# Optimization experiments

Hardware: AMD Instinct MI355X
Metric: run time of the kernel (lower is better)

The kernel has to match this reference:

```python
import jax, jax.numpy as jnp
import numpy as np

NA, NW = 131072, 131072
N = NA + NW
E = 1048576
R = 4
DIN = 64
H = 128
L = 2
EPS = 1e-5


def setup_inputs() -> dict:
    key = jax.random.key(0)
    ks = jax.random.split(key, 20)
    s_in = 1.0 / np.sqrt(DIN)
    s_h = 1.0 / np.sqrt(H)
    return {
        "x_assignments": jax.random.normal(ks[0], (NA, DIN), jnp.float32),
        "x_workers": jax.random.normal(ks[1], (NW, DIN), jnp.float32),
        "edge_index": jax.random.randint(ks[2], (2, E), 0, N),
        "edge_type": jax.random.randint(ks[3], (E,), 0, R),
        "W_in_a": jax.random.normal(ks[4], (DIN, H), jnp.float32) * s_in,
        "b_in_a": jnp.zeros((H,), jnp.float32),
        "W_in_w": jax.random.normal(ks[5], (DIN, H), jnp.float32) * s_in,
        "b_in_w": jnp.zeros((H,), jnp.float32),
        "W_rel": jax.random.normal(ks[6], (L, R, H, H), jnp.float32) * s_h,
        "W_root": jax.random.normal(ks[7], (L, H, H), jnp.float32) * s_h,
        "b_conv": jnp.zeros((L, H), jnp.float32),
        "ln_g": jnp.ones((L, H), jnp.float32),
        "ln_b": jnp.zeros((L, H), jnp.float32),
        "W_out": jax.random.normal(ks[8], (H, 1), jnp.float32) * s_h,
        "b_out": jnp.zeros((1,), jnp.float32),
        "base": jnp.zeros((), jnp.float32),
    }


def _layernorm(x, g, b):
    mu = jnp.mean(x, axis=-1, keepdims=True)
    var = jnp.var(x, axis=-1, keepdims=True)
    return (x - mu) * jax.lax.rsqrt(var + EPS) * g + b


def reference(x_assignments, x_workers, edge_index, edge_type,
              W_in_a, b_in_a, W_in_w, b_in_w,
              W_rel, W_root, b_conv, ln_g, ln_b,
              W_out, b_out, base):
    # type-specific input projection + relu, then flatten node space
    ha = jax.nn.relu(x_assignments @ W_in_a + b_in_a)
    hw = jax.nn.relu(x_workers @ W_in_w + b_in_w)
    h = jnp.concatenate([ha, hw], axis=0)  # [N, H]
    src, dst = edge_index[0], edge_index[1]
    for l in range(L):
        hs = h[src]  # [E, H] gathered source features
        out = h @ W_root[l] + b_conv[l]  # root transform + bias
        for r in range(R):
            m = (edge_type == r).astype(h.dtype)  # [E]
            agg = jax.ops.segment_sum(hs * m[:, None], dst, num_segments=N)
            cnt = jax.ops.segment_sum(m, dst, num_segments=N)
            mean = agg / jnp.maximum(cnt, 1.0)[:, None]  # per-relation mean aggr
            out = out + mean @ W_rel[l, r]
        h = jax.nn.relu(_layernorm(out, ln_g[l], ln_b[l]))
        # dropout inactive (eval mode)
    h_t = h[:NA]  # target node type slice (offset 0)
    pred = base + (h_t @ W_out + b_out)[:, 0]
    return pred
```

## Files before the change

### kernel.cpp

```cpp
#include <hip/hip_runtime.h>

#define NA_ 131072
#define NN  262144
#define EE  1048576
#define RR  4
#define EPS_ 1e-5f

typedef unsigned short ushort_t;
typedef unsigned char uchar_t;
typedef unsigned int uint_t;
typedef __attribute__((ext_vector_type(8))) short bf16x8;
typedef __attribute__((ext_vector_type(4))) float f32x4;

__device__ __forceinline__ float bf2f(uint_t u16) {
    return __uint_as_float(u16 << 16);
}
__device__ __forceinline__ uint_t f2bf(float f) {
    uint_t x = __float_as_uint(f);
    return (x + 0x7fffu + ((x >> 16) & 1u)) >> 16;
}

__device__ __forceinline__ void gl2lds16(const void* g, void* l) {
    __builtin_amdgcn_global_load_lds(
        (const __attribute__((address_space(1))) void*)g,
        (__attribute__((address_space(3))) void*)l, 16, 0, 0);
}
__device__ __forceinline__ void gl2lds16_nt(const void* g, void* l) {
    __builtin_amdgcn_global_load_lds(
        (const __attribute__((address_space(1))) void*)g,
        (__attribute__((address_space(3))) void*)l, 16, 0, 2);
}

__global__ __launch_bounds__(256) void proj_gemm(const float* __restrict__ A,
                                                 const short* __restrict__ Btg,
                                                 const float* __restrict__ bias,
                                                 ushort_t* __restrict__ C) {
    const int K = 64;
    __shared__ short As[128][K + 8];
    __shared__ short Bs[128][K + 8];
    const int tid  = threadIdx.x;
    const int lane = tid & 63;
    const int l15  = lane & 15;
    const int q    = lane >> 4;
    const int wv   = tid >> 6;
    const int wr   = (wv >> 1) * 64;
    const int wc   = (wv & 1) * 64;
    const size_t blockRow = (size_t)blockIdx.x * 128;

    #pragma unroll
    for (int it = 0; it < 4; it++) {
        int sidx = (it * 256 + tid) * 8;
        int row = sidx / K, col = sidx % K;
        const float* Ag = A + (blockRow + row) * K + col;
        float4 v0 = *(const float4*)Ag;
        float4 v1 = *(const float4*)(Ag + 4);
        uint4 u;
        u.x = f2bf(v0.x) | (f2bf(v0.y) << 16);
        u.y = f2bf(v0.z) | (f2bf(v0.w) << 16);
        u.z = f2bf(v1.x) | (f2bf(v1.y) << 16);
        u.w = f2bf(v1.z) | (f2bf(v1.w) << 16);
        *(uint4*)&As[row][col] = u;
        *(uint4*)&Bs[row][col] = *(const uint4*)(Btg + (size_t)row * K + col);
    }
    __syncthreads();

    f32x4 acc[4][4];
    #pragma unroll
    for (int i = 0; i < 4; i++)
        #pragma unroll
        for (int j = 0; j < 4; j++) {
            acc[i][j][0] = 0.f; acc[i][j][1] = 0.f;
            acc[i][j][2] = 0.f; acc[i][j][3] = 0.f;
        }

    #pragma unroll
    for (int kk = 0; kk < 2; kk++) {
        bf16x8 af[4], bfr[4];
        #pragma unroll
        for (int i = 0; i < 4; i++)
            af[i] = *(const bf16x8*)&As[wr + i * 16 + l15][kk * 32 + q * 8];
        #pragma unroll
        for (int j = 0; j < 4; j++)
            bfr[j] = *(const bf16x8*)&Bs[wc + j * 16 + l15][kk * 32 + q * 8];
        #pragma unroll
        for (int i = 0; i < 4; i++)
            #pragma unroll
            for (int j = 0; j < 4; j++)
                acc[i][j] = __builtin_amdgcn_mfma_f32_16x16x32_bf16(
                    af[i], bfr[j], acc[i][j], 0, 0, 0);
    }

    #pragma unroll
    for (int j = 0; j < 4; j++) {
        int gcol = wc + j * 16 + l15;
        float bv = bias[gcol];
        #pragma unroll
        for (int i = 0; i < 4; i++) {
            size_t rbase = blockRow + wr + i * 16 + q * 4;
            #pragma unroll
            for (int r = 0; r < 4; r++) {
                float v = fmaxf(acc[i][j][r] + bv, 0.f);
                C[(rbase + r) * 128 + gcol] = (ushort_t)f2bf(v);
            }
        }
    }
}

__global__ void prep_weights(const float* __restrict__ Wia,
                             const float* __restrict__ Wiw,
                             const float* __restrict__ Wroot,
                             const float* __restrict__ Wrel,
                             short* __restrict__ wt) {
    int e = blockIdx.x * 256 + threadIdx.x;
    if (e < 8192) {
        int k = e >> 7, n = e & 127;
        wt[n * 64 + k] = (short)f2bf(Wia[e]);
    } else if (e < 16384) {
        int t = e - 8192;
        int k = t >> 7, n = t & 127;
        wt[8192 + n * 64 + k] = (short)f2bf(Wiw[t]);
    } else {
        int t = e - 16384;
        int l = t / 81920;
        int d = t % 81920;
        int kc = d / 16384;
        int rem2 = d % 16384;
        int n = rem2 >> 7;
        int kkk = rem2 & 127;
        float val = (kc < 4)
            ? Wrel[(((size_t)l * 4 + kc) * 128 + kkk) * 128 + n]
            : Wroot[((size_t)l * 128 + kkk) * 128 + n];
        wt[16384 + (size_t)l * 81920 + kc * 16384 + n * 128 + kkk] =
            (short)f2bf(val);
    }
}

__global__ void count_edges(const int* __restrict__ dstv,
                            const int* __restrict__ et,
                            uint_t* __restrict__ cntp,
                            uchar_t* __restrict__ rank) {
    int base = blockIdx.x * 1024 + threadIdx.x;
    int e0 = base, e1 = base + 256, e2 = base + 512, e3 = base + 768;
    int r0 = et[e0], r1 = et[e1], r2 = et[e2], r3 = et[e3];
    int d0 = dstv[e0], d1 = dstv[e1], d2 = dstv[e2], d3 = dstv[e3];
    uint_t o0 = atomicAdd(&cntp[(size_t)d0 * 16], 1u << (8 * r0));
    uint_t o1 = atomicAdd(&cntp[(size_t)d1 * 16], 1u << (8 * r1));
    uint_t o2 = atomicAdd(&cntp[(size_t)d2 * 16], 1u << (8 * r2));
    uint_t o3 = atomicAdd(&cntp[(size_t)d3 * 16], 1u << (8 * r3));
    rank[e0] = (uchar_t)((o0 >> (8 * r0)) & 0xffu);
    rank[e1] = (uchar_t)((o1 >> (8 * r1)) & 0xffu);
    rank[e2] = (uchar_t)((o2 >> (8 * r2)) & 0xffu);
    rank[e3] = (uchar_t)((o3 >> (8 * r3)) & 0xffu);
}

__global__ void inv_deg(const uint_t* __restrict__ cntp,
                        float* __restrict__ inv,
                        int* __restrict__ deg,
                        uint_t* __restrict__ prefd) {
    int i = blockIdx.x * 256 + threadIdx.x;
    if (i < NN) {
        uint_t c = cntp[(size_t)i * 16];
        int c0 = c & 255, c1 = (c >> 8) & 255, c2 = (c >> 16) & 255, c3 = c >> 24;
        float4 w;
        w.x = 1.0f / (float)(c0 > 1 ? c0 : 1);
        w.y = 1.0f / (float)(c1 > 1 ? c1 : 1);
        w.z = 1.0f / (float)(c2 > 1 ? c2 : 1);
        w.w = 1.0f / (float)(c3 > 1 ? c3 : 1);
        ((float4*)inv)[i] = w;
        deg[i] = c0 + c1 + c2 + c3;
        prefd[i] = ((uint_t)c0 << 8) | ((uint_t)(c0 + c1) << 16)
                 | ((uint_t)(c0 + c1 + c2) << 24);
    }
}

__global__ void scan1(const int* __restrict__ deg, int* __restrict__ offs,
                      int* __restrict__ bsum) {
    __shared__ int lds[256];
    int tid = threadIdx.x;
    int i = blockIdx.x * 256 + tid;
    int v = deg[i];
    int incl = v;
    lds[tid] = incl;
    __syncthreads();
    for (int off = 1; off < 256; off <<= 1) {
        int t = (tid >= off) ? lds[tid - off] : 0;
        __syncthreads();
        incl += t;
        lds[tid] = incl;
        __syncthreads();
    }
    offs[i] = incl - v;
    if (tid == 255) bsum[blockIdx.x] = incl;
}

__global__ void scan_bsum(int* __restrict__ bsum) {
    __shared__ int lds[256];
    int tid = threadIdx.x;
    int t0 = bsum[tid * 4 + 0], t1 = bsum[tid * 4 + 1];
    int t2 = bsum[tid * 4 + 2], t3 = bsum[tid * 4 + 3];
    int s = t0 + t1 + t2 + t3;
    int incl = s;
    lds[tid] = incl;
    __syncthreads();
    for (int off = 1; off < 256; off <<= 1) {
        int t = (tid >= off) ? lds[tid - off] : 0;
        __syncthreads();
        incl += t;
        lds[tid] = incl;
        __syncthreads();
    }
    int e = incl - s;
    bsum[tid * 4 + 0] = e;
    bsum[tid * 4 + 1] = e + t0;
    bsum[tid * 4 + 2] = e + t0 + t1;
    bsum[tid * 4 + 3] = e + t0 + t1 + t2;
}

__global__ void scan_add(int* __restrict__ offs, const int* __restrict__ bsum) {
    int i = blockIdx.x * 256 + threadIdx.x;
    offs[i] = offs[i] + bsum[blockIdx.x];
    if (i == 0) offs[NN] = EE;
}

__global__ void place_edges(const int* __restrict__ srcv,
                            const int* __restrict__ dstv,
                            const int* __restrict__ et,
                            const uchar_t* __restrict__ rank,
                            const int* __restrict__ offs,
                            const uint_t* __restrict__ prefd,
                            uint_t* __restrict__ pk) {
    int base = blockIdx.x * 1024 + threadIdx.x;
    #pragma unroll
    for (int t = 0; t < 4; t++) {
        int e = base + t * 256;
        int d = dstv[e], r = et[e];
        int pos = offs[d] + (int)((prefd[d] >> (8 * r)) & 255u) + (int)rank[e];
        pk[pos] = (uint_t)srcv[e] | ((uint_t)r << 18);
    }
}

__global__ __launch_bounds__(256) void agg_means(const uint_t* __restrict__ pk,
                                                 const int* __restrict__ offs,
                                                 const ushort_t* __restrict__ hold,
                                                 const float* __restrict__ inv,
                                                 ushort_t* __restrict__ M,
                                                 int lo, int rowsCap) {
    const int wv  = __builtin_amdgcn_readfirstlane(threadIdx.x >> 6);
    const int idx = blockIdx.x * 4 + wv;
    const int d   = lo + idx;
    const int lane = threadIdx.x & 63;
    const int beg = offs[d];
    const int end = offs[d + 1];
    const float4 w4 = ((const float4*)inv)[d];

    float a0x = 0.f, a0y = 0.f, a1x = 0.f, a1y = 0.f;
    float a2x = 0.f, a2y = 0.f, a3x = 0.f, a3y = 0.f;

    const uint_t* hold32 = (const uint_t*)hold;

    auto accs = [&](uint_t p, uint_t v, bool valid) {
        float x = bf2f(v & 0xffffu), y = bf2f(v >> 16);
        uint_t r = p >> 18;
        float m0 = (valid && r == 0u) ? 1.f : 0.f;
        float m1 = (valid && r == 1u) ? 1.f : 0.f;
        float m2 = (valid && r == 2u) ? 1.f : 0.f;
        float m3 = (valid && r == 3u) ? 1.f : 0.f;
        a0x += m0 * x;  a0y += m0 * y;
        a1x += m1 * x;  a1y += m1 * y;
        a2x += m2 * x;  a2y += m2 * y;
        a3x += m3 * x;  a3y += m3 * y;
    };

    for (int e = beg; e < end; e += 8) {
        const int last = end - 1;
        int a1i = (e + 1 < end) ? e + 1 : last;
        int a2i = (e + 2 < end) ? e + 2 : last;
        int a3i = (e + 3 < end) ? e + 3 : last;
        uint_t p0 = pk[e];
        uint_t p1 = pk[a1i];
        uint_t p2 = pk[a2i];
        uint_t p3 = pk[a3i];
        uint_t v0 = hold32[(size_t)(p0 & 0x3FFFFu) * 64 + lane];
        uint_t v1 = hold32[(size_t)(p1 & 0x3FFFFu) * 64 + lane];
        uint_t v2 = hold32[(size_t)(p2 & 0x3FFFFu) * 64 + lane];
        uint_t v3 = hold32[(size_t)(p3 & 0x3FFFFu) * 64 + lane];

        const bool hB = (e + 4 < end);
        if (hB) {
            int b1i = (e + 5 < end) ? e + 5 : last;
            int b2i = (e + 6 < end) ? e + 6 : last;
            int b3i = (e + 7 < end) ? e + 7 : last;
            uint_t q0 = pk[e + 4];
            uint_t q1 = pk[b1i];
            uint_t q2 = pk[b2i];
            uint_t q3 = pk[b3i];
            uint_t u0 = hold32[(size_t)(q0 & 0x3FFFFu) * 64 + lane];
            uint_t u1 = hold32[(size_t)(q1 & 0x3FFFFu) * 64 + lane];
            uint_t u2 = hold32[(size_t)(q2 & 0x3FFFFu) * 64 + lane];
            uint_t u3 = hold32[(size_t)(q3 & 0x3FFFFu) * 64 + lane];
            accs(p0, v0, true);
            accs(p1, v1, true);
            accs(p2, v2, true);
            accs(p3, v3, true);
            accs(q0, u0, true);
            accs(q1, u1, e + 5 < end);
            accs(q2, u2, e + 6 < end);
            accs(q3, u3, e + 7 < end);
        } else {
            accs(p0, v0, true);
            accs(p1, v1, e + 1 < end);
            accs(p2, v2, e + 2 < end);
            accs(p3, v3, e + 3 < end);
        }
    }

    uint_t* P = (uint_t*)M;
    size_t planeU = (size_t)rowsCap * 64;
    size_t rowU = (size_t)idx * 64 + lane;
    __builtin_nontemporal_store(
        f2bf(a0x * w4.x) | (f2bf(a0y * w4.x) << 16), &P[rowU]);
    __builtin_nontemporal_store(
        f2bf(a1x * w4.y) | (f2bf(a1y * w4.y) << 16), &P[planeU + rowU]);
    __builtin_nontemporal_store(
        f2bf(a2x * w4.z) | (f2bf(a2y * w4.z) << 16), &P[2 * planeU + rowU]);
    __builtin_nontemporal_store(
        f2bf(a3x * w4.w) | (f2bf(a3y * w4.w) << 16), &P[3 * planeU + rowU]);
}

template<bool HEAD>
__global__ __launch_bounds__(256) void layer_gemm_ln(
    const ushort_t* __restrict__ Mg,
    const ushort_t* __restrict__ hold,
    const short* __restrict__ Btg,
    const float* __restrict__ bconv,
    const float* __restrict__ lng,
    const float* __restrict__ lnb,
    ushort_t* __restrict__ hnew,
    const float* __restrict__ Wout,
    const float* __restrict__ bout,
    const float* __restrict__ basep,
    float* __restrict__ pred,
    int lo, int rowsCap) {
    __shared__ short As[64 * 128];
    __shared__ short Bs[128 * 128];
    __shared__ float lds_s[64][2], lds_q[64][2], lds_h[64][2];

    const int tid  = threadIdx.x;
    const int lane = tid & 63;
    const int l15  = lane & 15;
    const int q    = lane >> 4;
    const int wv   = tid >> 6;
    const int wr   = (wv >> 1) * 32;
    const int wc   = (wv & 1) * 64;
    const int blockRowL = blockIdx.x * 64;
    const size_t planeS = (size_t)rowsCap * 128;

    f32x4 acc[2][4];
    #pragma unroll
    for (int i = 0; i < 2; i++)
        #pragma unroll
        for (int j = 0; j < 4; j++) {
            acc[i][j][0] = 0.f; acc[i][j][1] = 0.f;
            acc[i][j][2] = 0.f; acc[i][j][3] = 0.f;
        }

    const int rloc = lane >> 4;
    const int gsw  = (lane & 15) ^ ((wv * 4 + rloc) & 15);
    const int lby  = (rloc << 8) + (gsw << 4);

    for (int kc = 0; kc < 5; kc++) {
        const char* asrc = (kc < 4)
            ? (const char*)(Mg + (size_t)kc * planeS + (size_t)blockRowL * 128)
            : (const char*)(hold + (size_t)(lo + blockRowL) * 128);
        const char* bsrc = (const char*)(Btg + (size_t)kc * 16384);
        __syncthreads();
        #pragma unroll
        for (int it = 0; it < 8; it++) {
            int off = it * 4096 + wv * 1024;
            if (it < 4) {
                if (kc < 4) gl2lds16_nt(asrc + off + lby, (char*)As + off);
                else        gl2lds16(asrc + off + lby, (char*)As + off);
            }
            gl2lds16(bsrc + off + lby, (char*)Bs + off);
        }
        __syncthreads();

        #pragma unroll
        for (int kk = 0; kk < 4; kk++) {
            bf16x8 af[2], bfr[4];
            #pragma unroll
            for (int i = 0; i < 2; i++)
                af[i] = *(const bf16x8*)
                    &As[(wr + i * 16 + l15) * 128 + (((kk * 4 + q) ^ l15) << 3)];
            #pragma unroll
            for (int j = 0; j < 4; j++)
                bfr[j] = *(const bf16x8*)
                    &Bs[(wc + j * 16 + l15) * 128 + (((kk * 4 + q) ^ l15) << 3)];
            #pragma unroll
            for (int i = 0; i < 2; i++)
                #pragma unroll
                for (int j = 0; j < 4; j++)
                    acc[i][j] = __builtin_amdgcn_mfma_f32_16x16x32_bf16(
                        af[i], bfr[j], acc[i][j], 0, 0, 0);
        }
    }

    float bj[4], gj[4], bbj[4], wj[4];
    #pragma unroll
    for (int j = 0; j < 4; j++) {
        int col = wc + j * 16 + l15;
        bj[j]  = bconv[col];
        gj[j]  = lng[col];
        bbj[j] = lnb[col];
        if (HEAD) wj[j] = Wout[col];
    }
    #pragma unroll
    for (int i = 0; i < 2; i++)
        #pragma unroll
        for (int j = 0; j < 4; j++)
            #pragma unroll
            for (int r = 0; r < 4; r++) acc[i][j][r] += bj[j];

    float ps[2][4], pq[2][4];
    #pragma unroll
    for (int i = 0; i < 2; i++)
        #pragma unroll
        for (int r = 0; r < 4; r++) {
            float s = 0.f, qq = 0.f;
            #pragma unroll
            for (int j = 0; j < 4; j++) {
                float v = acc[i][j][r];
                s += v;
                qq += v * v;
            }
            ps[i][r] = s;
            pq[i][r] = qq;
        }
    #pragma unroll
    for (int m = 1; m <= 8; m <<= 1)
        #pragma unroll
        for (int i = 0; i < 2; i++)
            #pragma unroll
            for (int r = 0; r < 4; r++) {
                ps[i][r] += __shfl_xor(ps[i][r], m);
                pq[i][r] += __shfl_xor(pq[i][r], m);
            }

    if (l15 == 0) {
        #pragma unroll
        for (int i = 0; i < 2; i++)
            #pragma unroll
            for (int r = 0; r < 4; r++) {
                int row = wr + i * 16 + q * 4 + r;
                lds_s[row][wv & 1] = ps[i][r];
                lds_q[row][wv & 1] = pq[i][r];
            }
    }
    __syncthreads();

    float hs[2][4];
    #pragma unroll
    for (int i = 0; i < 2; i++)
        #pragma unroll
        for (int r = 0; r < 4; r++) {
            int row = wr + i * 16 + q * 4 + r;
            float sum = lds_s[row][0] + lds_s[row][1];
            float sq  = lds_q[row][0] + lds_q[row][1];
            float mu  = sum * (1.0f / 128.0f);
            float var = sq * (1.0f / 128.0f) - mu * mu;
            float rs  = rsqrtf(var + EPS_);
            size_t gr = (size_t)(lo + blockRowL + row) * 128;
            float hd = 0.f;
            #pragma unroll
            for (int j = 0; j < 4; j++) {
                float v = (acc[i][j][r] - mu) * rs * gj[j] + bbj[j];
                v = fmaxf(v, 0.f);
                if (HEAD) hd += v * wj[j];
                else hnew[gr + wc + j * 16 + l15] = (ushort_t)f2bf(v);
            }
            if (HEAD) hs[i][r] = hd;
        }

    if (HEAD) {
        #pragma unroll
        for (int m = 1; m <= 8; m <<= 1)
            #pragma unroll
            for (int i = 0; i < 2; i++)
                #pragma unroll
                for (int r = 0; r < 4; r++)
                    hs[i][r] += __shfl_xor(hs[i][r], m);
        if (l15 == 0) {
            #pragma unroll
            for (int i = 0; i < 2; i++)
                #pragma unroll
                for (int r = 0; r < 4; r++) {
                    int row = wr + i * 16 + q * 4 + r;
                    lds_h[row][wv & 1] = hs[i][r];
                }
        }
        __syncthreads();
        if (tid < 64)
            pred[lo + blockRowL + tid] =
                lds_h[tid][0] + lds_h[tid][1] + bout[0] + basep[0];
    }
}

extern "C" void kernel_launch(void* const* d_in, const int* in_sizes, int n_in,
                              void* d_out, int out_size, void* d_ws, size_t ws_size,
                              hipStream_t stream) {
    const float* x_a    = (const float*)d_in[0];
    const float* x_w    = (const float*)d_in[1];
    const int*   eidx   = (const int*)d_in[2];
    const int*   etype  = (const int*)d_in[3];
    const float* W_in_a = (const float*)d_in[4];
    const float* b_in_a = (const float*)d_in[5];
    const float* W_in_w = (const float*)d_in[6];
    const float* b_in_w = (const float*)d_in[7];
    const float* W_rel  = (const float*)d_in[8];
    const float* W_root = (const float*)d_in[9];
    const float* b_conv = (const float*)d_in[10];
    const float* ln_g   = (const float*)d_in[11];
    const float* ln_b   = (const float*)d_in[12];
    const float* W_out  = (const float*)d_in[13];
    const float* b_out  = (const float*)d_in[14];
    const float* base   = (const float*)d_in[15];

    const int* src  = eidx;
    const int* dstv = eidx + EE;

    char* p = (char*)d_ws;
    auto alloc = [&](size_t bytes) {
        char* q = p;
        p += (bytes + 255) & ~(size_t)255;
        return q;
    };
    ushort_t* hB   = (ushort_t*)alloc((size_t)NN * 128 * 2);
    float*    inv  = (float*)alloc((size_t)RR * NN * 4);
    uint_t*   pk   = (uint_t*)alloc((size_t)EE * 4);
    int*      offs = (int*)alloc((size_t)(NN + 1) * 4);
    short*    wbuf = (short*)alloc((size_t)180224 * 2);
    char*     hA_region = p;
    ushort_t* hA   = (ushort_t*)alloc((size_t)NN * 128 * 2);
    char*     scratch = p;
    uint_t*   cntp  = (uint_t*)alloc((size_t)NN * 64);
    uchar_t*  rank  = (uchar_t*)alloc((size_t)EE);
    int*      deg   = (int*)alloc((size_t)NN * 4);
    uint_t*   prefd = (uint_t*)alloc((size_t)NN * 4);
    int*      bsum  = (int*)alloc((size_t)1024 * 4);

    size_t rem0 = (ws_size > (size_t)(scratch - (char*)d_ws))
                      ? (ws_size - (size_t)(scratch - (char*)d_ws)) : 0;
    int cap0 = (int)(rem0 / 1024);
    if (cap0 > NN) cap0 = NN;
    cap0 &= ~127;
    if (cap0 == 0) cap0 = 128;
    size_t rem1 = (ws_size > (size_t)(hA_region - (char*)d_ws))
                      ? (ws_size - (size_t)(hA_region - (char*)d_ws)) : 0;
    int cap1 = (int)(rem1 / 1024);
    if (cap1 > NA_) cap1 = NA_;
    cap1 &= ~127;
    if (cap1 == 0) cap1 = 128;

    short* wt_ina = wbuf;
    short* wt_inw = wbuf + 8192;
    auto wt_layer = [&](int l) { return wbuf + 16384 + (size_t)l * 81920; };

    hipMemsetAsync(cntp, 0, (size_t)NN * 64, stream);
    count_edges<<<EE / 1024, 256, 0, stream>>>(dstv, etype, cntp, rank);
    inv_deg<<<NN / 256, 256, 0, stream>>>(cntp, inv, deg, prefd);
    scan1<<<NN / 256, 256, 0, stream>>>(deg, offs, bsum);
    scan_bsum<<<1, 256, 0, stream>>>(bsum);
    scan_add<<<NN / 256, 256, 0, stream>>>(offs, bsum);
    place_edges<<<EE / 1024, 256, 0, stream>>>(src, dstv, etype, rank, offs,
                                               prefd, pk);

    prep_weights<<<704, 256, 0, stream>>>(W_in_a, W_in_w, W_root, W_rel, wbuf);

    proj_gemm<<<NA_ / 128, 256, 0, stream>>>(x_a, wt_ina, b_in_a, hA);
    proj_gemm<<<NA_ / 128, 256, 0, stream>>>(x_w, wt_inw, b_in_w,
                                             hA + (size_t)NA_ * 128);

    ushort_t* hc = hA;
    ushort_t* hn = hB;
    for (int l = 0; l < 2; l++) {
        int Nout = (l == 0) ? NN : NA_;
        ushort_t* M = (l == 0) ? (ushort_t*)scratch : (ushort_t*)hA_region;
        int cap = (l == 0) ? cap0 : cap1;
        int nch = (Nout + cap - 1) / cap;
        int chunk = ((Nout / nch) + 127) & ~127;
        if (chunk > cap) chunk = cap;
        for (int lo = 0; lo < Nout; lo += chunk) {
            int cr = (Nout - lo < chunk) ? (Nout - lo) : chunk;
            agg_means<<<cr / 4, 256, 0, stream>>>(pk, offs, hc, inv, M, lo,
                                                  cap);
            if (l == 0)
                layer_gemm_ln<false><<<cr / 64, 256, 0, stream>>>(
                    M, hc, wt_layer(l), b_conv + l * 128, ln_g + l * 128,
                    ln_b + l * 128, hn, nullptr, nullptr, nullptr, nullptr,
                    lo, cap);
            else
                layer_gemm_ln<true><<<cr / 64, 256, 0, stream>>>(
                    M, hc, wt_layer(l), b_conv + l * 128, ln_g + l * 128,
                    ln_b + l * 128, nullptr, W_out, b_out, base,
                    (float*)d_out, lo, cap);
        }
        ushort_t* t = hc; hc = hn; hn = t;
    }
}
```

Measured before the change: 507.6 us.

## Fuse per-relation mean aggregation into layer GEMM+LayerNorm kernel via LDS

Replaces the separate agg_means kernel and its global bf16 M buffer with a fused 1024-thread kernel. Each wave aggregates 4 destination rows into LDS, then the block runs the 5-chunk MFMA GEMM with double-buffered weights and the LayerNorm/head epilogue. This removes the large global write and re-read of the aggregated means and the chunked launch loop. In exchange, LDS use per block rises sharply, limiting occupancy during the latency-bound gather phase.

```diff
diff --git a/kernel.cpp b/kernel.cpp
--- a/kernel.cpp
+++ b/kernel.cpp
@@ -24,11 +24,6 @@
     __builtin_amdgcn_global_load_lds(
         (const __attribute__((address_space(1))) void*)g,
         (__attribute__((address_space(3))) void*)l, 16, 0, 0);
-}
-__device__ __forceinline__ void gl2lds16_nt(const void* g, void* l) {
-    __builtin_amdgcn_global_load_lds(
-        (const __attribute__((address_space(1))) void*)g,
-        (__attribute__((address_space(3))) void*)l, 16, 0, 2);
 }
 
 __global__ __launch_bounds__(256) void proj_gemm(const float* __restrict__ A,
@@ -239,98 +234,12 @@
     }
 }
 
-__global__ __launch_bounds__(256) void agg_means(const uint_t* __restrict__ pk,
-                                                 const int* __restrict__ offs,
-                                                 const ushort_t* __restrict__ hold,
-                                                 const float* __restrict__ inv,
-                                                 ushort_t* __restrict__ M,
-                                                 int lo, int rowsCap) {
-    const int wv  = __builtin_amdgcn_readfirstlane(threadIdx.x >> 6);
-    const int idx = blockIdx.x * 4 + wv;
-    const int d   = lo + idx;
-    const int lane = threadIdx.x & 63;
-    const int beg = offs[d];
-    const int end = offs[d + 1];
-    const float4 w4 = ((const float4*)inv)[d];
-
-    float a0x = 0.f, a0y = 0.f, a1x = 0.f, a1y = 0.f;
-    float a2x = 0.f, a2y = 0.f, a3x = 0.f, a3y = 0.f;
-
-    const uint_t* hold32 = (const uint_t*)hold;
-
-    auto accs = [&](uint_t p, uint_t v, bool valid) {
-        float x = bf2f(v & 0xffffu), y = bf2f(v >> 16);
-        uint_t r = p >> 18;
-        float m0 = (valid && r == 0u) ? 1.f : 0.f;
-        float m1 = (valid && r == 1u) ? 1.f : 0.f;
-        float m2 = (valid && r == 2u) ? 1.f : 0.f;
-        float m3 = (valid && r == 3u) ? 1.f : 0.f;
-        a0x += m0 * x;  a0y += m0 * y;
-        a1x += m1 * x;  a1y += m1 * y;
-        a2x += m2 * x;  a2y += m2 * y;
-        a3x += m3 * x;  a3y += m3 * y;
-    };
-
-    for (int e = beg; e < end; e += 8) {
-        const int last = end - 1;
-        int a1i = (e + 1 < end) ? e + 1 : last;
-        int a2i = (e + 2 < end) ? e + 2 : last;
-        int a3i = (e + 3 < end) ? e + 3 : last;
-        uint_t p0 = pk[e];
-        uint_t p1 = pk[a1i];
-        uint_t p2 = pk[a2i];
-        uint_t p3 = pk[a3i];
-        uint_t v0 = hold32[(size_t)(p0 & 0x3FFFFu) * 64 + lane];
-        uint_t v1 = hold32[(size_t)(p1 & 0x3FFFFu) * 64 + lane];
-        uint_t v2 = hold32[(size_t)(p2 & 0x3FFFFu) * 64 + lane];
-        uint_t v3 = hold32[(size_t)(p3 & 0x3FFFFu) * 64 + lane];
-
-        const bool hB = (e + 4 < end);
-        if (hB) {
-            int b1i = (e + 5 < end) ? e + 5 : last;
-            int b2i = (e + 6 < end) ? e + 6 : last;
-            int b3i = (e + 7 < end) ? e + 7 : last;
-            uint_t q0 = pk[e + 4];
-            uint_t q1 = pk[b1i];
-            uint_t q2 = pk[b2i];
-            uint_t q3 = pk[b3i];
-            uint_t u0 = hold32[(size_t)(q0 & 0x3FFFFu) * 64 + lane];
-            uint_t u1 = hold32[(size_t)(q1 & 0x3FFFFu) * 64 + lane];
-            uint_t u2 = hold32[(size_t)(q2 & 0x3FFFFu) * 64 + lane];
-            uint_t u3 = hold32[(size_t)(q3 & 0x3FFFFu) * 64 + lane];
-            accs(p0, v0, true);
-            accs(p1, v1, true);
-            accs(p2, v2, true);
-            accs(p3, v3, true);
-            accs(q0, u0, true);
-            accs(q1, u1, e + 5 < end);
-            accs(q2, u2, e + 6 < end);
-            accs(q3, u3, e + 7 < end);
-        } else {
-            accs(p0, v0, true);
-            accs(p1, v1, e + 1 < end);
-            accs(p2, v2, e + 2 < end);
-            accs(p3, v3, e + 3 < end);
-        }
-    }
-
-    uint_t* P = (uint_t*)M;
-    size_t planeU = (size_t)rowsCap * 64;
-    size_t rowU = (size_t)idx * 64 + lane;
-    __builtin_nontemporal_store(
-        f2bf(a0x * w4.x) | (f2bf(a0y * w4.x) << 16), &P[rowU]);
-    __builtin_nontemporal_store(
-        f2bf(a1x * w4.y) | (f2bf(a1y * w4.y) << 16), &P[planeU + rowU]);
-    __builtin_nontemporal_store(
-        f2bf(a2x * w4.z) | (f2bf(a2y * w4.z) << 16), &P[2 * planeU + rowU]);
-    __builtin_nontemporal_store(
-        f2bf(a3x * w4.w) | (f2bf(a3y * w4.w) << 16), &P[3 * planeU + rowU]);
-}
-
 template<bool HEAD>
-__global__ __launch_bounds__(256) void layer_gemm_ln(
-    const ushort_t* __restrict__ Mg,
+__global__ __launch_bounds__(1024) void fused_layer(
+    const uint_t* __restrict__ pk,
+    const int* __restrict__ offs,
     const ushort_t* __restrict__ hold,
+    const float* __restrict__ inv,
     const short* __restrict__ Btg,
     const float* __restrict__ bconv,
     const float* __restrict__ lng,
@@ -339,169 +248,216 @@
     const float* __restrict__ Wout,
     const float* __restrict__ bout,
     const float* __restrict__ basep,
-    float* __restrict__ pred,
-    int lo, int rowsCap) {
+    float* __restrict__ pred) {
+    __shared__ short Ms[4 * 64 * 128];
     __shared__ short As[64 * 128];
-    __shared__ short Bs[128 * 128];
-    __shared__ float lds_s[64][2], lds_q[64][2], lds_h[64][2];
+    __shared__ short Bs[2 * 128 * 128];
+    __shared__ float lds_s[64][4], lds_q[64][4], lds_h[64][4];
 
     const int tid  = threadIdx.x;
     const int lane = tid & 63;
+    const int w    = __builtin_amdgcn_readfirstlane(tid >> 6);
     const int l15  = lane & 15;
     const int q    = lane >> 4;
-    const int wv   = tid >> 6;
-    const int wr   = (wv >> 1) * 32;
-    const int wc   = (wv & 1) * 64;
-    const int blockRowL = blockIdx.x * 64;
-    const size_t planeS = (size_t)rowsCap * 128;
-
-    f32x4 acc[2][4];
-    #pragma unroll
-    for (int i = 0; i < 2; i++)
-        #pragma unroll
-        for (int j = 0; j < 4; j++) {
-            acc[i][j][0] = 0.f; acc[i][j][1] = 0.f;
-            acc[i][j][2] = 0.f; acc[i][j][3] = 0.f;
-        }
+    const int baseRow = blockIdx.x * 64;
 
     const int rloc = lane >> 4;
-    const int gsw  = (lane & 15) ^ ((wv * 4 + rloc) & 15);
+    const int gsw  = (lane & 15) ^ ((w * 4 + rloc) & 15);
     const int lby  = (rloc << 8) + (gsw << 4);
 
-    for (int kc = 0; kc < 5; kc++) {
-        const char* asrc = (kc < 4)
-            ? (const char*)(Mg + (size_t)kc * planeS + (size_t)blockRowL * 128)
-            : (const char*)(hold + (size_t)(lo + blockRowL) * 128);
-        const char* bsrc = (const char*)(Btg + (size_t)kc * 16384);
-        __syncthreads();
-        #pragma unroll
-        for (int it = 0; it < 8; it++) {
-            int off = it * 4096 + wv * 1024;
-            if (it < 4) {
-                if (kc < 4) gl2lds16_nt(asrc + off + lby, (char*)As + off);
-                else        gl2lds16(asrc + off + lby, (char*)As + off);
+    {
+        const char* hsrc = (const char*)(hold + (size_t)baseRow * 128);
+        gl2lds16(hsrc + w * 1024 + lby, (char*)As + w * 1024);
+        const char* bsrc = (const char*)Btg;
+        gl2lds16(bsrc + w * 1024 + lby, (char*)Bs + w * 1024);
+        gl2lds16(bsrc + 16384 + w * 1024 + lby, (char*)Bs + 16384 + w * 1024);
+    }
+
+    const uint_t* hold32 = (const uint_t*)hold;
+    for (int s = 0; s < 4; ++s) {
+        const int row = w * 4 + s;
+        const int d   = baseRow + row;
+        const int beg = offs[d];
+        const int end = offs[d + 1];
+        const float4 w4 = ((const float4*)inv)[d];
+
+        float a0x = 0.f, a0y = 0.f, a1x = 0.f, a1y = 0.f;
+        float a2x = 0.f, a2y = 0.f, a3x = 0.f, a3y = 0.f;
+
+        auto accs = [&](uint_t p, uint_t v, bool valid) {
+            float x = bf2f(v & 0xffffu), y = bf2f(v >> 16);
+            uint_t r = p >> 18;
+            float m0 = (valid && r == 0u) ? 1.f : 0.f;
+            float m1 = (valid && r == 1u) ? 1.f : 0.f;
+            float m2 = (valid && r == 2u) ? 1.f : 0.f;
+            float m3 = (valid && r == 3u) ? 1.f : 0.f;
+            a0x += m0 * x;  a0y += m0 * y;
+            a1x += m1 * x;  a1y += m1 * y;
+            a2x += m2 * x;  a2y += m2 * y;
+            a3x += m3 * x;  a3y += m3 * y;
+        };
+
+        for (int e = beg; e < end; e += 8) {
+            const int last = end - 1;
+            int a1i = (e + 1 < end) ? e + 1 : last;
+            int a2i = (e + 2 < end) ? e + 2 : last;
+            int a3i = (e + 3 < end) ? e + 3 : last;
+            uint_t p0 = pk[e];
+            uint_t p1 = pk[a1i];
+            uint_t p2 = pk[a2i];
+            uint_t p3 = pk[a3i];
+            uint_t v0 = hold32[(size_t)(p0 & 0x3FFFFu) * 64 + lane];
+            uint_t v1 = hold32[(size_t)(p1 & 0x3FFFFu) * 64 + lane];
+            uint_t v2 = hold32[(size_t)(p2 & 0x3FFFFu) * 64 + lane];
+            uint_t v3 = hold32[(size_t)(p3 & 0x3FFFFu) * 64 + lane];
+
+            const bool hB2 = (e + 4 < end);
+            if (hB2) {
+                int b1i = (e + 5 < end) ? e + 5 : last;
+                int b2i = (e + 6 < end) ? e + 6 : last;
+                int b3i = (e + 7 < end) ? e + 7 : last;
+                uint_t q0 = pk[e + 4];
+                uint_t q1 = pk[b1i];
+                uint_t q2 = pk[b2i];
+                uint_t q3 = pk[b3i];
+                uint_t u0 = hold32[(size_t)(q0 & 0x3FFFFu) * 64 + lane];
+                uint_t u1 = hold32[(size_t)(q1 & 0x3FFFFu) * 64 + lane];
+                uint_t u2 = hold32[(size_t)(q2 & 0x3FFFFu) * 64 + lane];
+                uint_t u3 = hold32[(size_t)(q3 & 0x3FFFFu) * 64 + lane];
+                accs(p0, v0, true);
+                accs(p1, v1, true);
+                accs(p2, v2, true);
+                accs(p3, v3, true);
+                accs(q0, u0, true);
+                accs(q1, u1, e + 5 < end);
+                accs(q2, u2, e + 6 < end);
+                accs(q3, u3, e + 7 < end);
+            } else {
+                accs(p0, v0, true);
+                accs(p1, v1, e + 1 < end);
+                accs(p2, v2, e + 2 < end);
+                accs(p3, v3, e + 3 < end);
             }
-            gl2lds16(bsrc + off + lby, (char*)Bs + off);
-        }
-        __syncthreads();
-
-        #pragma unroll
-        for (int kk = 0; kk < 4; kk++) {
-            bf16x8 af[2], bfr[4];
+        }
+
+        char* mrow = (char*)Ms + row * 256
+                   + ((((lane >> 2) ^ (row & 15))) << 4) + (lane & 3) * 4;
+        *(uint_t*)(mrow)             = f2bf(a0x * w4.x) | (f2bf(a0y * w4.x) << 16);
+        *(uint_t*)(mrow + 16384)     = f2bf(a1x * w4.y) | (f2bf(a1y * w4.y) << 16);
+        *(uint_t*)(mrow + 2 * 16384) = f2bf(a2x * w4.z) | (f2bf(a2y * w4.z) << 16);
+        *(uint_t*)(mrow + 3 * 16384) = f2bf(a3x * w4.w) | (f2bf(a3y * w4.w) << 16);
+    }
+    __syncthreads();
+
+    const int wr16 = (w >> 2) * 16;
+    const int wcn  = (w & 3) * 32;
+    f32x4 acc[2];
+    acc[0][0] = 0.f; acc[0][1] = 0.f; acc[0][2] = 0.f; acc[0][3] = 0.f;
+    acc[1][0] = 0.f; acc[1][1] = 0.f; acc[1][2] = 0.f; acc[1][3] = 0.f;
+
+    for (int kc = 0; kc < 5; ++kc) {
+        if (kc < 4) {
+            const char* bn = (const char*)(Btg + (size_t)(kc + 1) * 16384);
+            char* bd = (char*)Bs + (((kc & 1) ^ 1)) * 32768;
+            gl2lds16(bn + w * 1024 + lby, bd + w * 1024);
+            gl2lds16(bn + 16384 + w * 1024 + lby, bd + 16384 + w * 1024);
+        }
+        const char* Asrc = (kc < 4) ? ((const char*)Ms + kc * 16384)
+                                    : (const char*)As;
+        const char* Bcur = (const char*)Bs + (kc & 1) * 32768;
+        #pragma unroll
+        for (int kk = 0; kk < 4; ++kk) {
+            const int g = (kk * 4 + q) ^ l15;
+            bf16x8 af = *(const bf16x8*)(Asrc + (wr16 + l15) * 256 + (g << 4));
             #pragma unroll
-            for (int i = 0; i < 2; i++)
-                af[i] = *(const bf16x8*)
-                    &As[(wr + i * 16 + l15) * 128 + (((kk * 4 + q) ^ l15) << 3)];
-            #pragma unroll
-            for (int j = 0; j < 4; j++)
-                bfr[j] = *(const bf16x8*)
-                    &Bs[(wc + j * 16 + l15) * 128 + (((kk * 4 + q) ^ l15) << 3)];
-            #pragma unroll
-            for (int i = 0; i < 2; i++)
-                #pragma unroll
-                for (int j = 0; j < 4; j++)
-                    acc[i][j] = __builtin_amdgcn_mfma_f32_16x16x32_bf16(
-                        af[i], bfr[j], acc[i][j], 0, 0, 0);
-        }
-    }
-
-    float bj[4], gj[4], bbj[4], wj[4];
-    #pragma unroll
-    for (int j = 0; j < 4; j++) {
-        int col = wc + j * 16 + l15;
+            for (int j = 0; j < 2; ++j) {
+                bf16x8 bf = *(const bf16x8*)
+                    (Bcur + (wcn + j * 16 + l15) * 256 + (g << 4));
+                acc[j] = __builtin_amdgcn_mfma_f32_16x16x32_bf16(
+                    af, bf, acc[j], 0, 0, 0);
+            }
+        }
+        if (kc < 4) __syncthreads();
+    }
+
+    float bj[2], gj[2], bbj[2], wj[2];
+    #pragma unroll
+    for (int j = 0; j < 2; ++j) {
+        int col = wcn + j * 16 + l15;
         bj[j]  = bconv[col];
         gj[j]  = lng[col];
         bbj[j] = lnb[col];
         if (HEAD) wj[j] = Wout[col];
     }
     #pragma unroll
-    for (int i = 0; i < 2; i++)
-        #pragma unroll
-        for (int j = 0; j < 4; j++)
-            #pragma unroll
-            for (int r = 0; r < 4; r++) acc[i][j][r] += bj[j];
-
-    float ps[2][4], pq[2][4];
-    #pragma unroll
-    for (int i = 0; i < 2; i++)
-        #pragma unroll
-        for (int r = 0; r < 4; r++) {
-            float s = 0.f, qq = 0.f;
-            #pragma unroll
-            for (int j = 0; j < 4; j++) {
-                float v = acc[i][j][r];
-                s += v;
-                qq += v * v;
-            }
-            ps[i][r] = s;
-            pq[i][r] = qq;
-        }
+    for (int j = 0; j < 2; ++j)
+        #pragma unroll
+        for (int r = 0; r < 4; ++r) acc[j][r] += bj[j];
+
+    float ps[4], pq[4];
+    #pragma unroll
+    for (int r = 0; r < 4; ++r) {
+        float v0 = acc[0][r], v1 = acc[1][r];
+        ps[r] = v0 + v1;
+        pq[r] = v0 * v0 + v1 * v1;
+    }
     #pragma unroll
     for (int m = 1; m <= 8; m <<= 1)
         #pragma unroll
-        for (int i = 0; i < 2; i++)
-            #pragma unroll
-            for (int r = 0; r < 4; r++) {
-                ps[i][r] += __shfl_xor(ps[i][r], m);
-                pq[i][r] += __shfl_xor(pq[i][r], m);
-            }
+        for (int r = 0; r < 4; ++r) {
+            ps[r] += __shfl_xor(ps[r], m);
+            pq[r] += __shfl_xor(pq[r], m);
+        }
 
     if (l15 == 0) {
         #pragma unroll
-        for (int i = 0; i < 2; i++)
-            #pragma unroll
-            for (int r = 0; r < 4; r++) {
-                int row = wr + i * 16 + q * 4 + r;
-                lds_s[row][wv & 1] = ps[i][r];
-                lds_q[row][wv & 1] = pq[i][r];
-            }
+        for (int r = 0; r < 4; ++r) {
+            int row = wr16 + q * 4 + r;
+            lds_s[row][w & 3] = ps[r];
+            lds_q[row][w & 3] = pq[r];
+        }
     }
     __syncthreads();
 
-    float hs[2][4];
-    #pragma unroll
-    for (int i = 0; i < 2; i++)
-        #pragma unroll
-        for (int r = 0; r < 4; r++) {
-            int row = wr + i * 16 + q * 4 + r;
-            float sum = lds_s[row][0] + lds_s[row][1];
-            float sq  = lds_q[row][0] + lds_q[row][1];
-            float mu  = sum * (1.0f / 128.0f);
-            float var = sq * (1.0f / 128.0f) - mu * mu;
-            float rs  = rsqrtf(var + EPS_);
-            size_t gr = (size_t)(lo + blockRowL + row) * 128;
-            float hd = 0.f;
-            #pragma unroll
-            for (int j = 0; j < 4; j++) {
-                float v = (acc[i][j][r] - mu) * rs * gj[j] + bbj[j];
-                v = fmaxf(v, 0.f);
-                if (HEAD) hd += v * wj[j];
-                else hnew[gr + wc + j * 16 + l15] = (ushort_t)f2bf(v);
-            }
-            if (HEAD) hs[i][r] = hd;
-        }
+    float hs[4];
+    #pragma unroll
+    for (int r = 0; r < 4; ++r) {
+        int row = wr16 + q * 4 + r;
+        float sum = lds_s[row][0] + lds_s[row][1] + lds_s[row][2] + lds_s[row][3];
+        float sq  = lds_q[row][0] + lds_q[row][1] + lds_q[row][2] + lds_q[row][3];
+        float mu  = sum * (1.0f / 128.0f);
+        float var = sq * (1.0f / 128.0f) - mu * mu;
+        float rs  = rsqrtf(var + EPS_);
+        size_t gr = (size_t)(baseRow + row) * 128;
+        float hd = 0.f;
+        #pragma unroll
+        for (int j = 0; j < 2; ++j) {
+            float v = (acc[j][r] - mu) * rs * gj[j] + bbj[j];
+            v = fmaxf(v, 0.f);
+            if (HEAD) hd += v * wj[j];
+            else hnew[gr + wcn + j * 16 + l15] = (ushort_t)f2bf(v);
+        }
+        if (HEAD) hs[r] = hd;
+    }
 
     if (HEAD) {
         #pragma unroll
         for (int m = 1; m <= 8; m <<= 1)
             #pragma unroll
-            for (int i = 0; i < 2; i++)
-                #pragma unroll
-                for (int r = 0; r < 4; r++)
-                    hs[i][r] += __shfl_xor(hs[i][r], m);
+            for (int r = 0; r < 4; ++r)
+                hs[r] += __shfl_xor(hs[r], m);
         if (l15 == 0) {
             #pragma unroll
-            for (int i = 0; i < 2; i++)
-                #pragma unroll
-                for (int r = 0; r < 4; r++) {
-                    int row = wr + i * 16 + q * 4 + r;
-                    lds_h[row][wv & 1] = hs[i][r];
-                }
+            for (int r = 0; r < 4; ++r) {
+                int row = wr16 + q * 4 + r;
+                lds_h[row][w & 3] = hs[r];
+            }
         }
         __syncthreads();
         if (tid < 64)
-            pred[lo + blockRowL + tid] =
-                lds_h[tid][0] + lds_h[tid][1] + bout[0] + basep[0];
+            pred[baseRow + tid] = lds_h[tid][0] + lds_h[tid][1]
+                                + lds_h[tid][2] + lds_h[tid][3]
+                                + bout[0] + basep[0];
     }
 }
 
@@ -539,27 +495,12 @@
     uint_t*   pk   = (uint_t*)alloc((size_t)EE * 4);
     int*      offs = (int*)alloc((size_t)(NN + 1) * 4);
     short*    wbuf = (short*)alloc((size_t)180224 * 2);
-    char*     hA_region = p;
     ushort_t* hA   = (ushort_t*)alloc((size_t)NN * 128 * 2);
-    char*     scratch = p;
     uint_t*   cntp  = (uint_t*)alloc((size_t)NN * 64);
     uchar_t*  rank  = (uchar_t*)alloc((size_t)EE);
     int*      deg   = (int*)alloc((size_t)NN * 4);
     uint_t*   prefd = (uint_t*)alloc((size_t)NN * 4);
     int*      bsum  = (int*)alloc((size_t)1024 * 4);
-
-    size_t rem0 = (ws_size > (size_t)(scratch - (char*)d_ws))
-                      ? (ws_size - (size_t)(scratch - (char*)d_ws)) : 0;
-    int cap0 = (int)(rem0 / 1024);
-    if (cap0 > NN) cap0 = NN;
-    cap0 &= ~127;
-    if (cap0 == 0) cap0 = 128;
-    size_t rem1 = (ws_size > (size_t)(hA_region - (char*)d_ws))
-                      ? (ws_size - (size_t)(hA_region - (char*)d_ws)) : 0;
-    int cap1 = (int)(rem1 / 1024);
-    if (cap1 > NA_) cap1 = NA_;
-    cap1 &= ~127;
-    if (cap1 == 0) cap1 = 128;
 
     short* wt_ina = wbuf;
     short* wt_inw = wbuf + 8192;
@@ -580,30 +521,10 @@
     proj_gemm<<<NA_ / 128, 256, 0, stream>>>(x_w, wt_inw, b_in_w,
                                              hA + (size_t)NA_ * 128);
 
-    ushort_t* hc = hA;
-    ushort_t* hn = hB;
-    for (int l = 0; l < 2; l++) {
-        int Nout = (l == 0) ? NN : NA_;
-        ushort_t* M = (l == 0) ? (ushort_t*)scratch : (ushort_t*)hA_region;
-        int cap = (l == 0) ? cap0 : cap1;
-        int nch = (Nout + cap - 1) / cap;
-        int chunk = ((Nout / nch) + 127) & ~127;
-        if (chunk > cap) chunk = cap;
-        for (int lo = 0; lo < Nout; lo += chunk) {
-            int cr = (Nout - lo < chunk) ? (Nout - lo) : chunk;
-            agg_means<<<cr / 4, 256, 0, stream>>>(pk, offs, hc, inv, M, lo,
-                                                  cap);
-            if (l == 0)
-                layer_gemm_ln<false><<<cr / 64, 256, 0, stream>>>(
-                    M, hc, wt_layer(l), b_conv + l * 128, ln_g + l * 128,
-                    ln_b + l * 128, hn, nullptr, nullptr, nullptr, nullptr,
-                    lo, cap);
-            else
-                layer_gemm_ln<true><<<cr / 64, 256, 0, stream>>>(
-                    M, hc, wt_layer(l), b_conv + l * 128, ln_g + l * 128,
-                    ln_b + l * 128, nullptr, W_out, b_out, base,
-                    (float*)d_out, lo, cap);
-        }
-        ushort_t* t = hc; hc = hn; hn = t;
-    }
-}
+    fused_layer<false><<<NN / 64, 1024, 0, stream>>>(
+        pk, offs, hA, inv, wt_layer(0), b_conv, ln_g, ln_b, hB,
+        nullptr, nullptr, nullptr, nullptr);
+    fused_layer<true><<<NA_ / 64, 1024, 0, stream>>>(
+        pk, offs, hB, inv, wt_layer(1), b_conv + 128, ln_g + 128, ln_b + 128,
+        nullptr, W_out, b_out, base, (float*)d_out);
+}
```

Result: slower. 543.5 us (+7.1%).
